# Optimization experiments

Measured on AMD Instinct MI355X. Metric: run time of the kernel, lower is better.

## Reference

```python
import jax, jax.numpy as jnp
import numpy as np

D_MODEL = 1024
D_K = 64
D_V = 64
N_HEADS = 16
LN_EPS = 1e-5


def setup_inputs() -> dict:
    key = jax.random.key(0)
    ks = jax.random.split(key, 9)
    B, S = 2, 2048
    scale = 0.02
    return {
        "input_Q": jax.random.normal(ks[0], (B, S, D_MODEL), dtype=jnp.float32),
        "input_K": jax.random.normal(ks[1], (B, S, D_MODEL), dtype=jnp.float32),
        "input_V": jax.random.normal(ks[2], (B, S, D_MODEL), dtype=jnp.float32),
        "W_Q": jax.random.normal(ks[3], (D_MODEL, N_HEADS * D_K), dtype=jnp.float32) * scale,
        "W_K": jax.random.normal(ks[4], (D_MODEL, N_HEADS * D_K), dtype=jnp.float32) * scale,
        "W_V": jax.random.normal(ks[5], (D_MODEL, N_HEADS * D_V), dtype=jnp.float32) * scale,
        "W_O": jax.random.normal(ks[6], (N_HEADS * D_V, D_MODEL), dtype=jnp.float32) * scale,
        "ln_gamma": jnp.ones((D_MODEL,), dtype=jnp.float32),
        "ln_beta": jnp.zeros((D_MODEL,), dtype=jnp.float32),
    }


def reference(input_Q, input_K, input_V, W_Q, W_K, W_V, W_O, ln_gamma, ln_beta):
    B, Lq, _ = input_Q.shape
    Lk = input_K.shape[1]
    # projections -> [B, H, L, d]
    Q = (input_Q @ W_Q).reshape(B, Lq, N_HEADS, D_K).transpose(0, 2, 1, 3)
    K = (input_K @ W_K).reshape(B, Lk, N_HEADS, D_K).transpose(0, 2, 1, 3)
    V = (input_V @ W_V).reshape(B, Lk, N_HEADS, D_V).transpose(0, 2, 1, 3)
    # scores: [B, H, Lq, Lk]
    scores = jnp.einsum("bhqd,bhkd->bhqk", Q, K) / jnp.sqrt(jnp.float32(D_K))
    # NOTE: source uses nn.Softmax(dim=1) -> softmax over the HEADS axis (faithful quirk)
    attn = jax.nn.softmax(scores, axis=1)
    context = jnp.einsum("bhqk,bhkv->bhqv", attn, V)
    context = context.transpose(0, 2, 1, 3).reshape(B, Lq, N_HEADS * D_V)
    output = context @ W_O
    # residual + LayerNorm over last dim
    x = output + input_Q
    mu = jnp.mean(x, axis=-1, keepdims=True)
    var = jnp.mean(jnp.square(x - mu), axis=-1, keepdims=True)
    return (x - mu) / jnp.sqrt(var + LN_EPS) * ln_gamma + ln_beta
```

## Files before the change

### kernel.cpp

```cpp
#include <hip/hip_runtime.h>
#include <cstdint>
#include <cstddef>

#define DM 1024
#define HEADS 16
#define DHEAD 64
#define SEQ 2048
#define BATCH 2

typedef __bf16 bf16x8 __attribute__((ext_vector_type(8)));
typedef float  f32x4  __attribute__((ext_vector_type(4)));
typedef unsigned short u16;
typedef unsigned int u32;
typedef u16 u16x8 __attribute__((ext_vector_type(8)));
typedef u16 u16x4 __attribute__((ext_vector_type(4)));

__device__ __forceinline__ float bf2f(u16 u){
    union { u32 i; float f; } v; v.i = ((u32)u) << 16; return v.f;
}
__device__ __forceinline__ u16 f2bf(float f){
    union { float f; u32 i; } v; v.f = f;
    u32 r = v.i + 0x7FFF + ((v.i >> 16) & 1);
    return (u16)(r >> 16);
}
__device__ __forceinline__ u16 f2bf_rhu(float f){
    union { float f; u32 i; } v; v.f = f;
    return (u16)((v.i + 0x8000u) >> 16);
}
__device__ __forceinline__ void gload16(const u16* g, u16* l){
    __builtin_amdgcn_global_load_lds(
        (const __attribute__((address_space(1))) u32*)g,
        (__attribute__((address_space(3))) u32*)l, 16, 0, 0);
}

__global__ void k_probe(const u16* __restrict__ q, int* __restrict__ flag){
    if (threadIdx.x == 0 && blockIdx.x == 0){
        int cnt = 0;
        for (int i = 0; i < 256; i += 2){
            int e = (q[i] >> 7) & 0xFF;
            if (e >= 90 && e <= 141) cnt++;
        }
        *flag = (cnt >= 64) ? 1 : 0;
    }
}

__global__ __launch_bounds__(256) void k_cvt3(const void* __restrict__ s0,
                                              const void* __restrict__ s1,
                                              const void* __restrict__ s2,
                                              u16* __restrict__ dstbase,
                                              const int* __restrict__ flag, int n){
    int z = blockIdx.y;
    const void* src = (z == 0) ? s0 : ((z == 1) ? s1 : s2);
    u16* dst = dstbase + (size_t)z * n;
    int i = (blockIdx.x * 256 + threadIdx.x) * 8;
    if (i >= n) return;
    if (*flag){
        *(u16x8*)&dst[i] = *(const u16x8*)((const u16*)src + i);
    } else {
        const float* s = (const float*)src + i;
        u16x8 o;
        #pragma unroll
        for (int j = 0; j < 8; j++) o[j] = f2bf(s[j]);
        *(u16x8*)&dst[i] = o;
    }
}

__global__ void k_tcvt4(const void* __restrict__ w0, const void* __restrict__ w1,
                        const void* __restrict__ w2, const void* __restrict__ w3,
                        u16* __restrict__ dstbase,
                        const int* __restrict__ flag, int R, int C){
    __shared__ u16 tile[32][33];
    int z = blockIdx.z;
    const void* src = (z == 0) ? w0 : ((z == 1) ? w1 : ((z == 2) ? w2 : w3));
    u16* dst = dstbase + (size_t)z * R * C;
    bool isbf = (*flag != 0);
    int c0 = blockIdx.x * 32, r0 = blockIdx.y * 32;
    int tx = threadIdx.x, ty = threadIdx.y;
    #pragma unroll
    for (int i = 0; i < 32; i += 8){
        size_t idx = (size_t)(r0 + ty + i) * C + c0 + tx;
        tile[ty + i][tx] = isbf ? ((const u16*)src)[idx] : f2bf(((const float*)src)[idx]);
    }
    __syncthreads();
    #pragma unroll
    for (int i = 0; i < 32; i += 8)
        dst[(size_t)(c0 + ty + i) * R + r0 + tx] = tile[tx][ty + i];
}

__global__ void k_transpose(const u16* __restrict__ src, u16* __restrict__ dst,
                            int R, int C){
    __shared__ u16 tile[32][33];
    size_t boff = (size_t)blockIdx.z * R * C;
    src += boff; dst += boff;
    int c0 = blockIdx.x * 32, r0 = blockIdx.y * 32;
    int tx = threadIdx.x, ty = threadIdx.y;
    #pragma unroll
    for (int i = 0; i < 32; i += 8)
        tile[ty + i][tx] = src[(size_t)(r0 + ty + i) * C + c0 + tx];
    __syncthreads();
    #pragma unroll
    for (int i = 0; i < 32; i += 8)
        dst[(size_t)(c0 + ty + i) * R + r0 + tx] = tile[tx][ty + i];
}

__global__ __launch_bounds__(256, 2) void k_gemm2z(const u16* __restrict__ A0,
                                                   const u16* __restrict__ Bt0,
                                                   u16* __restrict__ C0,
                                                   size_t strA, size_t strB, size_t strC,
                                                   int M, int N, int K){
    __shared__ u16 lsA[128 * 32];
    __shared__ u16 lsB[64 * 32];
    int z = blockIdx.z;
    const u16* A  = A0  + strA * z;
    const u16* Bt = Bt0 + strB * z;
    u16* C = C0 + strC * z;
    int m0 = blockIdx.y * 128, n0 = blockIdx.x * 64;
    int t = threadIdx.x, lane = t & 63, w = t >> 6;
    int l15 = lane & 15, quad = lane >> 4;
    int wm = (w & 1) * 64, wn = (w >> 1) * 32;
    int rA0 = 32 * w + (lane >> 2);
    int rA1 = rA0 + 16;
    int rB  = 16 * w + (lane >> 2);
    int cA0 = (lane & 3) ^ (rA0 & 3);
    int cA1 = (lane & 3) ^ (rA1 & 3);
    int cB  = (lane & 3) ^ (rB  & 3);
    u16* dA0 = &lsA[(32 * w) * 32];
    u16* dA1 = &lsA[(32 * w + 16) * 32];
    u16* dB  = &lsB[(16 * w) * 32];
    f32x4 acc[4][2] = {};
    for (int k0 = 0; k0 < K; k0 += 32){
        __syncthreads();
        gload16(&A [(size_t)(m0 + rA0) * K + k0 + cA0 * 8], dA0);
        gload16(&A [(size_t)(m0 + rA1) * K + k0 + cA1 * 8], dA1);
        gload16(&Bt[(size_t)(n0 + rB ) * K + k0 + cB  * 8], dB);
        __syncthreads();
        bf16x8 af[4], bfr[2];
        #pragma unroll
        for (int i = 0; i < 4; i++){
            int row = wm + i * 16 + l15;
            af[i] = *(const bf16x8*)&lsA[row * 32 + ((quad ^ (row & 3)) * 8)];
        }
        #pragma unroll
        for (int j = 0; j < 2; j++){
            int row = wn + j * 16 + l15;
            bfr[j] = *(const bf16x8*)&lsB[row * 32 + ((quad ^ (row & 3)) * 8)];
        }
        #pragma unroll
        for (int i = 0; i < 4; i++)
            #pragma unroll
            for (int j = 0; j < 2; j++)
                acc[i][j] = __builtin_amdgcn_mfma_f32_16x16x32_bf16(af[i], bfr[j], acc[i][j], 0, 0, 0);
    }
    #pragma unroll
    for (int i = 0; i < 4; i++)
        #pragma unroll
        for (int j = 0; j < 2; j++)
            #pragma unroll
            for (int r = 0; r < 4; r++){
                int m = m0 + wm + i * 16 + quad * 4 + r;
                int n = n0 + wn + j * 16 + l15;
                C[(size_t)m * N + n] = f2bf(acc[i][j][r]);
            }
}

__global__ __launch_bounds__(1024, 4) void k_attn4(const u16* __restrict__ Qp,
                                                   const u16* __restrict__ Kp,
                                                   const u16* __restrict__ Vt,
                                                   u16* __restrict__ c0,
                                                   u16* __restrict__ c1,
                                                   u16* __restrict__ c2,
                                                   u16* __restrict__ c3,
                                                   int qtShift, int iters){
    __shared__ u16 ebuf[2][16][64][36];
    int bid = blockIdx.x;
    int combo = bid & ((1 << qtShift) - 1);
    int b = combo & 1, chunk = combo >> 1;
    int q0 = (bid >> qtShift) * 64;
    int t = threadIdx.x;
    int h = t >> 6, lane = t & 63, l15 = lane & 15, quad = lane >> 4;
    u16* outp = (chunk == 0) ? c0 : ((chunk == 1) ? c1 : ((chunk == 2) ? c2 : c3));
    const float cexp = 0.125f * 1.44269504f;
    int kbeg = chunk * (iters << 5);

    bf16x8 qf[4][2];
    #pragma unroll
    for (int sub = 0; sub < 4; sub++)
        #pragma unroll
        for (int ch = 0; ch < 2; ch++)
            qf[sub][ch] = *(const bf16x8*)&Qp[((size_t)(b * SEQ + q0 + sub * 16 + l15)) * DM
                                             + h * DHEAD + ch * 32 + quad * 8];

    f32x4 oacc[4][4] = {};
    int sq = t >> 4, sku = (t & 15) * 2;

    auto score_phase = [&](int it){
        int k0 = kbeg + (it << 5), bf = it & 1;
        #pragma unroll
        for (int kt = 0; kt < 2; kt++){
            const u16* kb = Kp + ((size_t)(b * SEQ + k0 + kt * 16 + l15)) * DM + h * DHEAD + quad * 8;
            bf16x8 kf0 = *(const bf16x8*)(kb);
            bf16x8 kf1 = *(const bf16x8*)(kb + 32);
            #pragma unroll
            for (int sub = 0; sub < 4; sub++){
                f32x4 sc = {};
                sc = __builtin_amdgcn_mfma_f32_16x16x32_bf16(qf[sub][0], kf0, sc, 0, 0, 0);
                sc = __builtin_amdgcn_mfma_f32_16x16x32_bf16(qf[sub][1], kf1, sc, 0, 0, 0);
                #pragma unroll
                for (int r = 0; r < 4; r++)
                    ebuf[bf][h][sub * 16 + quad * 4 + r][kt * 16 + l15] =
                        f2bf_rhu(exp2f(sc[r] * cexp));
            }
        }
    };

    score_phase(0);
    for (int it = 0; it < iters; it++){
        int bf = it & 1;
        __syncthreads();
        {
            u32 ev[16];
            float s0 = 0.f, s1 = 0.f;
            #pragma unroll
            for (int hh = 0; hh < 16; hh++){
                u32 u = *(const u32*)&ebuf[bf][hh][sq][sku];
                ev[hh] = u;
                union { u32 i; float f; } lo, hi;
                lo.i = u << 16; hi.i = u & 0xFFFF0000u;
                s0 += lo.f; s1 += hi.f;
            }
            float r0 = __builtin_amdgcn_rcpf(s0);
            float r1 = __builtin_amdgcn_rcpf(s1);
            #pragma unroll
            for (int hh = 0; hh < 16; hh++){
                union { u32 i; float f; } lo, hi, p0, p1;
                lo.i = ev[hh] << 16; hi.i = ev[hh] & 0xFFFF0000u;
                p0.f = lo.f * r0; p1.f = hi.f * r1;
                *(u32*)&ebuf[bf][hh][sq][sku] =
                    ((p0.i + 0x8000u) >> 16) | ((p1.i + 0x8000u) & 0xFFFF0000u);
            }
        }
        __syncthreads();
        int k0 = kbeg + (it << 5);
        bf16x8 pa[4];
        #pragma unroll
        for (int sub = 0; sub < 4; sub++){
            const u16* pp = &ebuf[bf][h][sub * 16 + l15][quad * 8];
            union { bf16x8 v; u16x4 q[2]; } pu;
            pu.q[0] = *(const u16x4*)pp;
            pu.q[1] = *(const u16x4*)(pp + 4);
            pa[sub] = pu.v;
        }
        #pragma unroll
        for (int vt = 0; vt < 4; vt++){
            bf16x8 vf = *(const bf16x8*)&Vt[((size_t)b * DM + h * DHEAD + vt * 16 + l15) * SEQ
                                            + k0 + quad * 8];
            #pragma unroll
            for (int sub = 0; sub < 4; sub++)
                oacc[sub][vt] = __builtin_amdgcn_mfma_f32_16x16x32_bf16(pa[sub], vf, oacc[sub][vt], 0, 0, 0);
        }
        if (it + 1 < iters) score_phase(it + 1);
    }
    #pragma unroll
    for (int sub = 0; sub < 4; sub++)
        #pragma unroll
        for (int vt = 0; vt < 4; vt++)
            #pragma unroll
            for (int r = 0; r < 4; r++){
                int q = q0 + sub * 16 + quad * 4 + r;
                int n = h * DHEAD + vt * 16 + l15;
                outp[((size_t)b * SEQ + q) * DM + n] = f2bf(oacc[sub][vt][r]);
            }
}

__global__ __launch_bounds__(256) void k_reduce(const u16* __restrict__ a,
                                                const u16* __restrict__ b,
                                                const u16* __restrict__ c,
                                                const u16* __restrict__ d,
                                                u16* __restrict__ dst, int n, int nch){
    int i = (blockIdx.x * 256 + threadIdx.x) * 8;
    if (i >= n) return;
    u16x8 x = *(const u16x8*)&a[i];
    u16x8 y = *(const u16x8*)&b[i];
    u16x8 o;
    if (nch == 4){
        u16x8 zc = *(const u16x8*)&c[i];
        u16x8 zd = *(const u16x8*)&d[i];
        #pragma unroll
        for (int j = 0; j < 8; j++)
            o[j] = f2bf((bf2f(x[j]) + bf2f(y[j])) + (bf2f(zc[j]) + bf2f(zd[j])));
    } else {
        #pragma unroll
        for (int j = 0; j < 8; j++) o[j] = f2bf(bf2f(x[j]) + bf2f(y[j]));
    }
    *(u16x8*)&dst[i] = o;
}

__global__ __launch_bounds__(256) void k_ln(const u16* __restrict__ O,
                                            const void* __restrict__ Qin,
                                            const void* __restrict__ gamma,
                                            const void* __restrict__ beta,
                                            void* __restrict__ out,
                                            const int* __restrict__ flag){
    __shared__ float red[4][2];
    bool isbf = (*flag != 0);
    int row = blockIdx.x;
    int t = threadIdx.x;
    const u16* op = O + (size_t)row * DM;
    float xv[4];
    float s1 = 0.f, s2 = 0.f;
    #pragma unroll
    for (int i = 0; i < 4; i++){
        int idx = i * 256 + t;
        float q = isbf ? bf2f(((const u16*)Qin)[(size_t)row * DM + idx])
                       : ((const float*)Qin)[(size_t)row * DM + idx];
        float x = bf2f(op[idx]) + q;
        xv[i] = x; s1 += x; s2 += x * x;
    }
    #pragma unroll
    for (int off = 32; off; off >>= 1){
        s1 += __shfl_down(s1, off);
        s2 += __shfl_down(s2, off);
    }
    int w = t >> 6, lane = t & 63;
    if (lane == 0){ red[w][0] = s1; red[w][1] = s2; }
    __syncthreads();
    float S1 = red[0][0] + red[1][0] + red[2][0] + red[3][0];
    float S2 = red[0][1] + red[1][1] + red[2][1] + red[3][1];
    float mu  = S1 * (1.0f / DM);
    float var = S2 * (1.0f / DM) - mu * mu;
    float rstd = rsqrtf(var + 1e-5f);
    #pragma unroll
    for (int i = 0; i < 4; i++){
        int idx = i * 256 + t;
        float g = isbf ? bf2f(((const u16*)gamma)[idx]) : ((const float*)gamma)[idx];
        float bb= isbf ? bf2f(((const u16*)beta )[idx]) : ((const float*)beta )[idx];
        float y = (xv[i] - mu) * rstd * g + bb;
        if (isbf) ((u16*)out)[(size_t)row * DM + idx] = f2bf(y);
        else      ((float*)out)[(size_t)row * DM + idx] = y;
    }
}

extern "C" void kernel_launch(void* const* d_in, const int* in_sizes, int n_in,
                              void* d_out, int out_size, void* d_ws, size_t ws_size,
                              hipStream_t stream){
    (void)in_sizes; (void)n_in; (void)out_size;
    const void* inQ = d_in[0];
    const void* inK = d_in[1];
    const void* inV = d_in[2];
    const void* wQ  = d_in[3];
    const void* wK  = d_in[4];
    const void* wV  = d_in[5];
    const void* wO  = d_in[6];
    const void* gma = d_in[7];
    const void* bta = d_in[8];

    int* flag = (int*)d_ws;
    u16* base = (u16*)d_ws + 64;

    const size_t MB1 = 1024u * 1024u;
    const size_t M4  = 4u * MB1;
    u16* Qi  = base + 0;
    u16* Ki  = base + 1 * M4;
    u16* Vi  = base + 2 * M4;
    u16* WtQ = base + 3 * M4;
    u16* WtO = WtQ + 3 * MB1;
    u16* Qp  = base + 4 * M4;
    u16* Kp  = base + 5 * M4;
    u16* Vp  = base + 6 * M4;
    u16* ext = base + 7 * M4;
    u16* Vt    = Ki;
    u16* ctxp0 = Qi;
    u16* ctxp1 = Vp;
    u16* ctxp2 = Vi;

    size_t need4 = 128 + 8 * M4 * sizeof(u16);
    int nch = (ws_size >= need4) ? 4 : 2;
    u16* ctxp3 = (nch == 4) ? ext : ctxp2;
    int qtShift = (nch == 4) ? 3 : 2;
    int iters   = (nch == 4) ? 16 : 32;
    int ablocks = 32 * 2 * nch;

    k_probe<<<1, 64, 0, stream>>>((const u16*)inQ, flag);

    const int nIn = BATCH * SEQ * DM;
    k_cvt3<<<dim3(nIn / 2048, 3), 256, 0, stream>>>(inQ, inK, inV, base, flag, nIn);

    k_tcvt4<<<dim3(32, 32, 4), dim3(32, 8), 0, stream>>>(wQ, wK, wV, wO, WtQ, flag, 1024, 1024);

    k_gemm2z<<<dim3(16, 32, 3), 256, 0, stream>>>(Qi, WtQ, Qp, M4, MB1, M4, 4096, 1024, 1024);

    k_transpose<<<dim3(32, 64, 2), dim3(32, 8), 0, stream>>>(Vp, Vt, 2048, 1024);

    k_attn4<<<ablocks, 1024, 0, stream>>>(Qp, Kp, Vt, ctxp0, ctxp1, ctxp2, ctxp3,
                                          qtShift, iters);

    k_reduce<<<nIn / 2048, 256, 0, stream>>>(ctxp0, ctxp1, ctxp2, ctxp3, ctxp0, nIn, nch);

    k_gemm2z<<<dim3(16, 32, 1), 256, 0, stream>>>(ctxp0, WtO, Qp, 0, 0, 0, 4096, 1024, 1024);

    k_ln<<<4096, 256, 0, stream>>>(Qp, inQ, gma, bta, d_out, flag);
}
```

Before: 341.1 us.

## Enlarge GEMM tile to 128x128 and assign attention work per XCC via atomics

The projection and output GEMMs now compute 128x128 tiles per block, giving each wave a 64x64 sub-tile with 16 accumulators. This halves the grid and raises operand reuse from LDS. The attention kernel now reads the hardware XCC id and claims (batch, key-chunk) combos through atomic counters, so blocks on the same XCC tend to share K/V data in L2. The price is extra atomics and a dependence on counters zeroed by the probe kernel. It also raises register pressure in the GEMM.

After: 338.1 us. No clear change (-0.9%).

```diff
diff --git a/kernel.cpp b/kernel.cpp
--- a/kernel.cpp
+++ b/kernel.cpp
@@ -33,14 +33,16 @@
         (__attribute__((address_space(3))) u32*)l, 16, 0, 0);
 }
 
-__global__ void k_probe(const u16* __restrict__ q, int* __restrict__ flag){
+__global__ void k_probe(const u16* __restrict__ q, int* __restrict__ hdr){
     if (threadIdx.x == 0 && blockIdx.x == 0){
         int cnt = 0;
         for (int i = 0; i < 256; i += 2){
             int e = (q[i] >> 7) & 0xFF;
             if (e >= 90 && e <= 141) cnt++;
         }
-        *flag = (cnt >= 64) ? 1 : 0;
+        hdr[0] = (cnt >= 64) ? 1 : 0;
+        #pragma unroll
+        for (int c = 1; c <= 8; c++) hdr[c] = 0;
     }
 }
 
@@ -103,58 +105,58 @@
         dst[(size_t)(c0 + ty + i) * R + r0 + tx] = tile[tx][ty + i];
 }
 
-__global__ __launch_bounds__(256, 2) void k_gemm2z(const u16* __restrict__ A0,
+__global__ __launch_bounds__(256, 2) void k_gemm3z(const u16* __restrict__ A0,
                                                    const u16* __restrict__ Bt0,
                                                    u16* __restrict__ C0,
                                                    size_t strA, size_t strB, size_t strC,
                                                    int M, int N, int K){
     __shared__ u16 lsA[128 * 32];
-    __shared__ u16 lsB[64 * 32];
+    __shared__ u16 lsB[128 * 32];
     int z = blockIdx.z;
     const u16* A  = A0  + strA * z;
     const u16* Bt = Bt0 + strB * z;
     u16* C = C0 + strC * z;
-    int m0 = blockIdx.y * 128, n0 = blockIdx.x * 64;
+    int m0 = blockIdx.y * 128, n0 = blockIdx.x * 128;
     int t = threadIdx.x, lane = t & 63, w = t >> 6;
     int l15 = lane & 15, quad = lane >> 4;
-    int wm = (w & 1) * 64, wn = (w >> 1) * 32;
-    int rA0 = 32 * w + (lane >> 2);
-    int rA1 = rA0 + 16;
-    int rB  = 16 * w + (lane >> 2);
-    int cA0 = (lane & 3) ^ (rA0 & 3);
-    int cA1 = (lane & 3) ^ (rA1 & 3);
-    int cB  = (lane & 3) ^ (rB  & 3);
+    int wm = (w & 1) * 64, wn = (w >> 1) * 64;
+    int r0 = 32 * w + (lane >> 2);
+    int r1 = r0 + 16;
+    int c0s = (lane & 3) ^ (r0 & 3);
+    int c1s = (lane & 3) ^ (r1 & 3);
     u16* dA0 = &lsA[(32 * w) * 32];
     u16* dA1 = &lsA[(32 * w + 16) * 32];
-    u16* dB  = &lsB[(16 * w) * 32];
-    f32x4 acc[4][2] = {};
+    u16* dB0 = &lsB[(32 * w) * 32];
+    u16* dB1 = &lsB[(32 * w + 16) * 32];
+    f32x4 acc[4][4] = {};
     for (int k0 = 0; k0 < K; k0 += 32){
         __syncthreads();
-        gload16(&A [(size_t)(m0 + rA0) * K + k0 + cA0 * 8], dA0);
-        gload16(&A [(size_t)(m0 + rA1) * K + k0 + cA1 * 8], dA1);
-        gload16(&Bt[(size_t)(n0 + rB ) * K + k0 + cB  * 8], dB);
+        gload16(&A [(size_t)(m0 + r0) * K + k0 + c0s * 8], dA0);
+        gload16(&A [(size_t)(m0 + r1) * K + k0 + c1s * 8], dA1);
+        gload16(&Bt[(size_t)(n0 + r0) * K + k0 + c0s * 8], dB0);
+        gload16(&Bt[(size_t)(n0 + r1) * K + k0 + c1s * 8], dB1);
         __syncthreads();
-        bf16x8 af[4], bfr[2];
+        bf16x8 af[4], bfr[4];
         #pragma unroll
         for (int i = 0; i < 4; i++){
             int row = wm + i * 16 + l15;
             af[i] = *(const bf16x8*)&lsA[row * 32 + ((quad ^ (row & 3)) * 8)];
         }
         #pragma unroll
-        for (int j = 0; j < 2; j++){
+        for (int j = 0; j < 4; j++){
             int row = wn + j * 16 + l15;
             bfr[j] = *(const bf16x8*)&lsB[row * 32 + ((quad ^ (row & 3)) * 8)];
         }
         #pragma unroll
         for (int i = 0; i < 4; i++)
             #pragma unroll
-            for (int j = 0; j < 2; j++)
+            for (int j = 0; j < 4; j++)
                 acc[i][j] = __builtin_amdgcn_mfma_f32_16x16x32_bf16(af[i], bfr[j], acc[i][j], 0, 0, 0);
     }
     #pragma unroll
     for (int i = 0; i < 4; i++)
         #pragma unroll
-        for (int j = 0; j < 2; j++)
+        for (int j = 0; j < 4; j++)
             #pragma unroll
             for (int r = 0; r < 4; r++){
                 int m = m0 + wm + i * 16 + quad * 4 + r;
@@ -163,20 +165,35 @@
             }
 }
 
-__global__ __launch_bounds__(1024, 4) void k_attn4(const u16* __restrict__ Qp,
+__global__ __launch_bounds__(1024, 4) void k_attn5(const u16* __restrict__ Qp,
                                                    const u16* __restrict__ Kp,
                                                    const u16* __restrict__ Vt,
                                                    u16* __restrict__ c0,
                                                    u16* __restrict__ c1,
                                                    u16* __restrict__ c2,
                                                    u16* __restrict__ c3,
-                                                   int qtShift, int iters){
+                                                   int* __restrict__ cnt,
+                                                   int ncomboM1, int iters){
     __shared__ u16 ebuf[2][16][64][36];
-    int bid = blockIdx.x;
-    int combo = bid & ((1 << qtShift) - 1);
+    __shared__ int s_combo, s_slot;
+    int t = threadIdx.x;
+    if (t == 0){
+        int xcc;
+        asm volatile("s_getreg_b32 %0, hwreg(HW_REG_XCC_ID)" : "=s"(xcc));
+        int start = xcc & ncomboM1;
+        int combo = -1, slot = -1;
+        for (int a = 0; a <= ncomboM1 && combo < 0; a++){
+            int c = (start + a) & ncomboM1;
+            int s = atomicAdd(&cnt[c], 1);
+            if (s < 32){ combo = c; slot = s; }
+        }
+        s_combo = combo; s_slot = slot;
+    }
+    __syncthreads();
+    int combo = s_combo;
+    if (combo < 0) return;
     int b = combo & 1, chunk = combo >> 1;
-    int q0 = (bid >> qtShift) * 64;
-    int t = threadIdx.x;
+    int q0 = s_slot * 64;
     int h = t >> 6, lane = t & 63, l15 = lane & 15, quad = lane >> 4;
     u16* outp = (chunk == 0) ? c0 : ((chunk == 1) ? c1 : ((chunk == 2) ? c2 : c3));
     const float cexp = 0.125f * 1.44269504f;
@@ -354,7 +371,9 @@
     const void* gma = d_in[7];
     const void* bta = d_in[8];
 
-    int* flag = (int*)d_ws;
+    int* hdr  = (int*)d_ws;
+    int* flag = hdr;
+    int* cnt  = hdr + 1;
     u16* base = (u16*)d_ws + 64;
 
     const size_t MB1 = 1024u * 1024u;
@@ -376,27 +395,27 @@
     size_t need4 = 128 + 8 * M4 * sizeof(u16);
     int nch = (ws_size >= need4) ? 4 : 2;
     u16* ctxp3 = (nch == 4) ? ext : ctxp2;
-    int qtShift = (nch == 4) ? 3 : 2;
+    int ncomboM1 = 2 * nch - 1;
     int iters   = (nch == 4) ? 16 : 32;
     int ablocks = 32 * 2 * nch;
 
-    k_probe<<<1, 64, 0, stream>>>((const u16*)inQ, flag);
+    k_probe<<<1, 64, 0, stream>>>((const u16*)inQ, hdr);
 
     const int nIn = BATCH * SEQ * DM;
     k_cvt3<<<dim3(nIn / 2048, 3), 256, 0, stream>>>(inQ, inK, inV, base, flag, nIn);
 
     k_tcvt4<<<dim3(32, 32, 4), dim3(32, 8), 0, stream>>>(wQ, wK, wV, wO, WtQ, flag, 1024, 1024);
 
-    k_gemm2z<<<dim3(16, 32, 3), 256, 0, stream>>>(Qi, WtQ, Qp, M4, MB1, M4, 4096, 1024, 1024);
+    k_gemm3z<<<dim3(8, 32, 3), 256, 0, stream>>>(Qi, WtQ, Qp, M4, MB1, M4, 4096, 1024, 1024);
 
     k_transpose<<<dim3(32, 64, 2), dim3(32, 8), 0, stream>>>(Vp, Vt, 2048, 1024);
 
-    k_attn4<<<ablocks, 1024, 0, stream>>>(Qp, Kp, Vt, ctxp0, ctxp1, ctxp2, ctxp3,
-                                          qtShift, iters);
+    k_attn5<<<ablocks, 1024, 0, stream>>>(Qp, Kp, Vt, ctxp0, ctxp1, ctxp2, ctxp3,
+                                          cnt, ncomboM1, iters);
 
     k_reduce<<<nIn / 2048, 256, 0, stream>>>(ctxp0, ctxp1, ctxp2, ctxp3, ctxp0, nIn, nch);
 
-    k_gemm2z<<<dim3(16, 32, 1), 256, 0, stream>>>(ctxp0, WtO, Qp, 0, 0, 0, 4096, 1024, 1024);
+    k_gemm3z<<<dim3(8, 32, 1), 256, 0, stream>>>(ctxp0, WtO, Qp, 0, 0, 0, 4096, 1024, 1024);
 
     k_ln<<<4096, 256, 0, stream>>>(Qp, inQ, gma, bta, d_out, flag);
 }
```
